# Optimization experiments

Hardware: AMD Instinct MI355X
Metric: run time of the kernel (lower is better)

Reference implementation:

```python
import jax, jax.numpy as jnp
import numpy as np
from jax import lax

R = 1          # box-filter radius
EPS = 1e-06    # regularizer


def boxfilter(z, r=R):
    """ReplicationPad2d(r) + depthwise (groups=C) mean conv with kernel (2r+1)^2."""
    k = 2 * r + 1
    c = z.shape[1]
    zp = jnp.pad(z, ((0, 0), (0, 0), (r, r), (r, r)), mode='edge')  # replication pad
    w = jnp.full((c, 1, k, k), 1.0 / (k * k), dtype=z.dtype)        # [O, I/g, kh, kw]
    return lax.conv_general_dilated(zp, w, window_strides=(1, 1), padding='VALID',
                                    feature_group_count=c)


def setup_inputs() -> dict:
    key = jax.random.key(0)
    kx, ky = jax.random.split(key)
    shape = (8, 3, 1024, 1024)
    # image-valued inputs in [0, 255), matching the final clamp range
    x = jax.random.uniform(kx, shape, jnp.float32, 0.0, 255.0)
    y = jax.random.uniform(ky, shape, jnp.float32, 0.0, 255.0)
    return {"x": x, "y": y}


def reference(x, y):
    mean_x = boxfilter(x)
    mean_y = boxfilter(y)
    cov_xy = boxfilter(x * y) - mean_x * mean_y
    var_x = boxfilter(x * x) - mean_x * mean_x
    A = cov_xy / (var_x + EPS)
    b = mean_y - A * mean_x
    res = boxfilter(A) * x + boxfilter(b)
    # torch: res.int() truncates toward zero, clamp(0,255), back to float
    return jnp.clip(jnp.trunc(res), 0.0, 255.0)
```

## Files before the change

### kernel.cpp

```cpp
#include <hip/hip_runtime.h>


typedef float f4 __attribute__((ext_vector_type(4)));
typedef float f2 __attribute__((ext_vector_type(2)));

#define TH 16
#define OW 256

struct Row { f2 xl; f4 xm; f2 xr; f2 yl; f4 ym; f2 yr; };

__global__ __launch_bounds__(256) void gf_kernel(
    const float* __restrict__ xg, const float* __restrict__ yg,
    float* __restrict__ outg, int H, int W) {
  const int lane = threadIdx.x;
  const int img = blockIdx.z;
  const size_t ibase = (size_t)img * H * W;
  const float* __restrict__ xi = xg + ibase;
  const float* __restrict__ yi = yg + ibase;
  float* __restrict__ oi = outg + ibase;

  const int tx0 = blockIdx.x * OW;
  const int ty0 = (blockIdx.y * 4 + threadIdx.y) * TH;
  const int o0 = tx0 + 4 * lane;
  const bool fixl = (o0 == 0);
  const bool fixr = (o0 == W - 4);
  const int olo = fixl ? 0 : (o0 - 2);
  const int ohi = fixr ? (W - 2) : (o0 + 4);
  const float inv9 = 1.0f / 9.0f;

  Row r0, r1, r2, pf;
  f4 hA0, hA1, hA2, hA3, hB0, hB1, hB2, hB3;
  int nextr;

  auto ldrow = [&](int rr, Row& R) {
    const float* xr = xi + (size_t)rr * W;
    const float* yr = yi + (size_t)rr * W;
    R.xm = *(const f4*)(xr + o0);
    R.xl = *(const f2*)(xr + olo);
    R.xr = *(const f2*)(xr + ohi);
    R.ym = *(const f4*)(yr + o0);
    R.yl = *(const f2*)(yr + olo);
    R.yr = *(const f2*)(yr + ohi);
    if (fixl) { R.xl[1] = R.xl[0]; R.yl[1] = R.yl[0]; }
    if (fixr) { R.xr[0] = R.xr[1]; R.yr[0] = R.yr[1]; }
  };

  auto emit_row = [&](int ly, f4 xv) {
    f4 SA = hA1 + hA2 + hA3;
    f4 SB = hB1 + hB2 + hB3;
    f4 st;
#pragma unroll
    for (int j = 0; j < 4; ++j) {
      float res = (SA[j] * xv[j] + SB[j]) * inv9;
      float t = truncf(res);
      st[j] = fminf(fmaxf(t, 0.0f), 255.0f);
    }
    int gr = ty0 + ly - 2;
    __builtin_nontemporal_store(st, (f4*)(oi + (size_t)gr * W + o0));
  };

  auto dup_hist = [&]() {
    hA0 = hA1; hA1 = hA2; hA2 = hA3;
    hB0 = hB1; hB1 = hB2; hB2 = hB3;
  };

  auto step_adv = [&](int ly, bool doemit, bool dopf) {
    r0 = r1; r1 = r2; r2 = pf;
    if (dopf) {
      ldrow(nextr, pf);
      nextr = min(nextr + 1, H - 1);
    }
    f2 vxl = r0.xl + r1.xl + r2.xl;
    f4 vxm = r0.xm + r1.xm + r2.xm;
    f2 vxr = r0.xr + r1.xr + r2.xr;
    f2 vyl = r0.yl + r1.yl + r2.yl;
    f4 vym = r0.ym + r1.ym + r2.ym;
    f2 vyr = r0.yr + r1.yr + r2.yr;
    f2 vxyl = r0.xl * r0.yl + r1.xl * r1.yl + r2.xl * r2.yl;
    f4 vxym = r0.xm * r0.ym + r1.xm * r1.ym + r2.xm * r2.ym;
    f2 vxyr = r0.xr * r0.yr + r1.xr * r1.yr + r2.xr * r2.yr;
    f2 vxxl = r0.xl * r0.xl + r1.xl * r1.xl + r2.xl * r2.xl;
    f4 vxxm = r0.xm * r0.xm + r1.xm * r1.xm + r2.xm * r2.xm;
    f2 vxxr = r0.xr * r0.xr + r1.xr * r1.xr + r2.xr * r2.xr;
    float vx[8]  = {vxl[0],  vxl[1],  vxm[0],  vxm[1],  vxm[2],  vxm[3],  vxr[0],  vxr[1]};
    float vy[8]  = {vyl[0],  vyl[1],  vym[0],  vym[1],  vym[2],  vym[3],  vyr[0],  vyr[1]};
    float vxy[8] = {vxyl[0], vxyl[1], vxym[0], vxym[1], vxym[2], vxym[3], vxyr[0], vxyr[1]};
    float vxx[8] = {vxxl[0], vxxl[1], vxxm[0], vxxm[1], vxxm[2], vxxm[3], vxxr[0], vxxr[1]};
    float A[6], B[6];
#pragma unroll
    for (int j = 0; j < 6; ++j) {
      float Sx  = vx[j] + vx[j + 1] + vx[j + 2];
      float Sy  = vy[j] + vy[j + 1] + vy[j + 2];
      float Sxy = vxy[j] + vxy[j + 1] + vxy[j + 2];
      float Sxx = vxx[j] + vxx[j + 1] + vxx[j + 2];
      float num = 9.0f * Sxy - Sx * Sy;
      float den = 9.0f * Sxx - Sx * Sx + 8.1e-05f;
      float rd;
      asm("v_rcp_f32 %0, %1" : "=v"(rd) : "v"(den));
      float a = num * rd;
      A[j] = a;
      B[j] = Sy * inv9 - a * (Sx * inv9);
    }
    if (fixl) { A[0] = A[1]; B[0] = B[1]; }
    if (fixr) { A[5] = A[4]; B[5] = B[4]; }
    f4 hAn, hBn;
#pragma unroll
    for (int j = 0; j < 4; ++j) {
      hAn[j] = A[j] + A[j + 1] + A[j + 2];
      hBn[j] = B[j] + B[j + 1] + B[j + 2];
    }
    hA0 = hA1; hA1 = hA2; hA2 = hA3; hA3 = hAn;
    hB0 = hB1; hB1 = hB2; hB2 = hB3; hB3 = hBn;
    if (doemit) emit_row(ly, r0.xm);
  };

  {
    int cy0 = max(ty0 - 1, 0);
    int ra = max(cy0 - 1, 0);
    ldrow(ra, r1);
    ldrow(cy0, r2);
    nextr = min(cy0 + 1, H - 1);
    ldrow(nextr, pf);
    nextr = min(nextr + 1, H - 1);
  }
  hA0 = hA1 = hA2 = hA3 = (f4)(0.0f);
  hB0 = hB1 = hB2 = hB3 = (f4)(0.0f);

  step_adv(0, false, true);
  if (ty0 == 0) dup_hist();
  else step_adv(1, false, true);
#pragma unroll 4
  for (int ly = 2; ly <= TH; ++ly) step_adv(ly, true, true);
  if (ty0 == H - TH) {
    dup_hist();
    emit_row(TH + 1, r1.xm);
  } else {
    step_adv(TH + 1, true, false);
  }
}

extern "C" void kernel_launch(void* const* d_in, const int* in_sizes, int n_in,
                              void* d_out, int out_size, void* d_ws, size_t ws_size,
                              hipStream_t stream) {
  const float* x = (const float*)d_in[0];
  const float* y = (const float*)d_in[1];
  float* out = (float*)d_out;
  const int H = 1024, W = 1024;
  const int imgs = in_sizes[0] / (H * W);
  dim3 block(64, 4, 1);
  dim3 grid(W / OW, H / (TH * 4), imgs);
  gf_kernel<<<grid, block, 0, stream>>>(x, y, out, H, W);
}
```

Measured before the change: 248.6 us.

## Share horizontal halo via wavefront shuffles instead of extra halo loads

Each lane now loads only its own aligned float4 per row and gets neighbouring column sums through __shfl_up/__shfl_down, instead of issuing two extra float2 halo loads per input per row. Tiles overlap by one float4 on each side (OW 248, 62 output lanes per wave), so edge lanes compute halo and do not store, and the last block is clamped into range. Launch bounds now request higher occupancy and the 1/9 scaling of B is moved into the final emit. The cost is redundant compute on the two edge lanes, more blocks, and cross-lane shuffle latency.

```diff
diff --git a/kernel.cpp b/kernel.cpp
--- a/kernel.cpp
+++ b/kernel.cpp
@@ -2,14 +2,11 @@
 
 
 typedef float f4 __attribute__((ext_vector_type(4)));
-typedef float f2 __attribute__((ext_vector_type(2)));
 
 #define TH 16
-#define OW 256
+#define OW 248
 
-struct Row { f2 xl; f4 xm; f2 xr; f2 yl; f4 ym; f2 yr; };
-
-__global__ __launch_bounds__(256) void gf_kernel(
+__global__ __launch_bounds__(256, 6) void gf_kernel(
     const float* __restrict__ xg, const float* __restrict__ yg,
     float* __restrict__ outg, int H, int W) {
   const int lane = threadIdx.x;
@@ -19,30 +16,27 @@
   const float* __restrict__ yi = yg + ibase;
   float* __restrict__ oi = outg + ibase;
 
-  const int tx0 = blockIdx.x * OW;
+  int tx0 = blockIdx.x * OW;
+  const int skipb = tx0;
+  if (tx0 > W - OW) tx0 = W - OW;
   const int ty0 = (blockIdx.y * 4 + threadIdx.y) * TH;
-  const int o0 = tx0 + 4 * lane;
-  const bool fixl = (o0 == 0);
-  const bool fixr = (o0 == W - 4);
-  const int olo = fixl ? 0 : (o0 - 2);
-  const int ohi = fixr ? (W - 2) : (o0 + 4);
+
+  const int c0 = tx0 - 4 + 4 * lane;
+  const int ccl = min(max(c0, 0), W - 4);
+  const bool wok = (lane >= 1) && (lane <= 62) && (c0 >= skipb);
+  const bool fixl = (c0 == 0);
+  const bool fixr = (c0 == W - 4);
   const float inv9 = 1.0f / 9.0f;
 
-  Row r0, r1, r2, pf;
-  f4 hA0, hA1, hA2, hA3, hB0, hB1, hB2, hB3;
+  f4 x0, x1, x2, y0, y1, y2, xp, yp;
+  f4 hA1, hA2, hA3, hB1, hB2, hB3;
   int nextr;
 
-  auto ldrow = [&](int rr, Row& R) {
+  auto ldrow = [&](int rr, f4& xv, f4& yv) {
     const float* xr = xi + (size_t)rr * W;
     const float* yr = yi + (size_t)rr * W;
-    R.xm = *(const f4*)(xr + o0);
-    R.xl = *(const f2*)(xr + olo);
-    R.xr = *(const f2*)(xr + ohi);
-    R.ym = *(const f4*)(yr + o0);
-    R.yl = *(const f2*)(yr + olo);
-    R.yr = *(const f2*)(yr + ohi);
-    if (fixl) { R.xl[1] = R.xl[0]; R.yl[1] = R.yl[0]; }
-    if (fixr) { R.xr[0] = R.xr[1]; R.yr[0] = R.yr[1]; }
+    xv = *(const f4*)(xr + ccl);
+    yv = *(const f4*)(yr + ccl);
   };
 
   auto emit_row = [&](int ly, f4 xv) {
@@ -51,55 +45,67 @@
     f4 st;
 #pragma unroll
     for (int j = 0; j < 4; ++j) {
-      float res = (SA[j] * xv[j] + SB[j]) * inv9;
+      float res = (SA[j] * xv[j] + SB[j] * inv9) * inv9;
       float t = truncf(res);
       st[j] = fminf(fmaxf(t, 0.0f), 255.0f);
     }
-    int gr = ty0 + ly - 2;
-    __builtin_nontemporal_store(st, (f4*)(oi + (size_t)gr * W + o0));
+    if (wok) {
+      int gr = ty0 + ly - 2;
+      __builtin_nontemporal_store(st, (f4*)(oi + (size_t)gr * W + c0));
+    }
   };
 
   auto dup_hist = [&]() {
-    hA0 = hA1; hA1 = hA2; hA2 = hA3;
-    hB0 = hB1; hB1 = hB2; hB2 = hB3;
+    hA1 = hA2; hA2 = hA3;
+    hB1 = hB2; hB2 = hB3;
   };
 
   auto step_adv = [&](int ly, bool doemit, bool dopf) {
-    r0 = r1; r1 = r2; r2 = pf;
+    x0 = x1; x1 = x2; x2 = xp;
+    y0 = y1; y1 = y2; y2 = yp;
     if (dopf) {
-      ldrow(nextr, pf);
+      ldrow(nextr, xp, yp);
       nextr = min(nextr + 1, H - 1);
     }
-    f2 vxl = r0.xl + r1.xl + r2.xl;
-    f4 vxm = r0.xm + r1.xm + r2.xm;
-    f2 vxr = r0.xr + r1.xr + r2.xr;
-    f2 vyl = r0.yl + r1.yl + r2.yl;
-    f4 vym = r0.ym + r1.ym + r2.ym;
-    f2 vyr = r0.yr + r1.yr + r2.yr;
-    f2 vxyl = r0.xl * r0.yl + r1.xl * r1.yl + r2.xl * r2.yl;
-    f4 vxym = r0.xm * r0.ym + r1.xm * r1.ym + r2.xm * r2.ym;
-    f2 vxyr = r0.xr * r0.yr + r1.xr * r1.yr + r2.xr * r2.yr;
-    f2 vxxl = r0.xl * r0.xl + r1.xl * r1.xl + r2.xl * r2.xl;
-    f4 vxxm = r0.xm * r0.xm + r1.xm * r1.xm + r2.xm * r2.xm;
-    f2 vxxr = r0.xr * r0.xr + r1.xr * r1.xr + r2.xr * r2.xr;
-    float vx[8]  = {vxl[0],  vxl[1],  vxm[0],  vxm[1],  vxm[2],  vxm[3],  vxr[0],  vxr[1]};
-    float vy[8]  = {vyl[0],  vyl[1],  vym[0],  vym[1],  vym[2],  vym[3],  vyr[0],  vyr[1]};
-    float vxy[8] = {vxyl[0], vxyl[1], vxym[0], vxym[1], vxym[2], vxym[3], vxyr[0], vxyr[1]};
-    float vxx[8] = {vxxl[0], vxxl[1], vxxm[0], vxxm[1], vxxm[2], vxxm[3], vxxr[0], vxxr[1]};
+    f4 v[4];
+    v[0] = x0 + x1 + x2;
+    v[1] = y0 + y1 + y2;
+    v[2] = x0 * y0 + x1 * y1 + x2 * y2;
+    v[3] = x0 * x0 + x1 * x1 + x2 * x2;
+    float e[4][4];
+#pragma unroll
+    for (int q = 0; q < 4; ++q) {
+      e[q][0] = __shfl_up(v[q][2], 1);
+      e[q][1] = __shfl_up(v[q][3], 1);
+      e[q][2] = __shfl_down(v[q][0], 1);
+      e[q][3] = __shfl_down(v[q][1], 1);
+    }
+    if (fixl) {
+#pragma unroll
+      for (int q = 0; q < 4; ++q) { e[q][0] = v[q][0]; e[q][1] = v[q][0]; }
+    }
+    if (fixr) {
+#pragma unroll
+      for (int q = 0; q < 4; ++q) { e[q][2] = v[q][3]; e[q][3] = v[q][3]; }
+    }
+    float wx[8]  = {e[0][0], e[0][1], v[0][0], v[0][1], v[0][2], v[0][3], e[0][2], e[0][3]};
+    float wy[8]  = {e[1][0], e[1][1], v[1][0], v[1][1], v[1][2], v[1][3], e[1][2], e[1][3]};
+    float wxy[8] = {e[2][0], e[2][1], v[2][0], v[2][1], v[2][2], v[2][3], e[2][2], e[2][3]};
+    float wxx[8] = {e[3][0], e[3][1], v[3][0], v[3][1], v[3][2], v[3][3], e[3][2], e[3][3]};
     float A[6], B[6];
 #pragma unroll
     for (int j = 0; j < 6; ++j) {
-      float Sx  = vx[j] + vx[j + 1] + vx[j + 2];
-      float Sy  = vy[j] + vy[j + 1] + vy[j + 2];
-      float Sxy = vxy[j] + vxy[j + 1] + vxy[j + 2];
-      float Sxx = vxx[j] + vxx[j + 1] + vxx[j + 2];
+      float Sx  = wx[j] + wx[j + 1] + wx[j + 2];
+      float Sy  = wy[j] + wy[j + 1] + wy[j + 2];
+      float Sxy = wxy[j] + wxy[j + 1] + wxy[j + 2];
+      float Sxx = wxx[j] + wxx[j + 1] + wxx[j + 2];
       float num = 9.0f * Sxy - Sx * Sy;
       float den = 9.0f * Sxx - Sx * Sx + 8.1e-05f;
       float rd;
       asm("v_rcp_f32 %0, %1" : "=v"(rd) : "v"(den));
       float a = num * rd;
       A[j] = a;
-      B[j] = Sy * inv9 - a * (Sx * inv9);
+      B[j] = Sy - a * Sx;
     }
     if (fixl) { A[0] = A[1]; B[0] = B[1]; }
     if (fixr) { A[5] = A[4]; B[5] = B[4]; }
@@ -109,22 +115,22 @@
       hAn[j] = A[j] + A[j + 1] + A[j + 2];
       hBn[j] = B[j] + B[j + 1] + B[j + 2];
     }
-    hA0 = hA1; hA1 = hA2; hA2 = hA3; hA3 = hAn;
-    hB0 = hB1; hB1 = hB2; hB2 = hB3; hB3 = hBn;
-    if (doemit) emit_row(ly, r0.xm);
+    hA1 = hA2; hA2 = hA3; hA3 = hAn;
+    hB1 = hB2; hB2 = hB3; hB3 = hBn;
+    if (doemit) emit_row(ly, x0);
   };
 
   {
     int cy0 = max(ty0 - 1, 0);
     int ra = max(cy0 - 1, 0);
-    ldrow(ra, r1);
-    ldrow(cy0, r2);
+    ldrow(ra, x1, y1);
+    ldrow(cy0, x2, y2);
     nextr = min(cy0 + 1, H - 1);
-    ldrow(nextr, pf);
+    ldrow(nextr, xp, yp);
     nextr = min(nextr + 1, H - 1);
   }
-  hA0 = hA1 = hA2 = hA3 = (f4)(0.0f);
-  hB0 = hB1 = hB2 = hB3 = (f4)(0.0f);
+  hA1 = hA2 = hA3 = (f4)(0.0f);
+  hB1 = hB2 = hB3 = (f4)(0.0f);
 
   step_adv(0, false, true);
   if (ty0 == 0) dup_hist();
@@ -133,7 +139,7 @@
   for (int ly = 2; ly <= TH; ++ly) step_adv(ly, true, true);
   if (ty0 == H - TH) {
     dup_hist();
-    emit_row(TH + 1, r1.xm);
+    emit_row(TH + 1, x1);
   } else {
     step_adv(TH + 1, true, false);
   }
@@ -148,6 +154,6 @@
   const int H = 1024, W = 1024;
   const int imgs = in_sizes[0] / (H * W);
   dim3 block(64, 4, 1);
-  dim3 grid(W / OW, H / (TH * 4), imgs);
+  dim3 grid((W + OW - 1) / OW, H / (TH * 4), imgs);
   gf_kernel<<<grid, block, 0, stream>>>(x, y, out, H, W);
 }
```

Result: slower. 470.0 us (+89.1%).
